# Performance work log

Measured on AMD Instinct MI355X. Metric: run time of the kernel, lower is better.

Reference implementation:

```python
import jax, jax.numpy as jnp
import numpy as np

D = 128        # node/time feature dim (n_node_features)
E = 20         # edge feature dim (hard-coded in TGS)
N = 4096       # number of source nodes
K = 10         # neighbors per node (hard-coded n_neighbors=10)
NUM_NODES = 100000
NUM_EDGES = 500000


def setup_inputs() -> dict:
    key = jax.random.key(0)
    ks = jax.random.split(key, 11)
    node_features = jax.random.normal(ks[0], (NUM_NODES, D), jnp.float32)
    edge_features = jax.random.normal(ks[1], (NUM_EDGES, E), jnp.float32)
    source_nodes = jax.random.randint(ks[2], (N,), 0, NUM_NODES)
    timestamps = jax.random.uniform(ks[3], (N,), jnp.float32) * 1000.0
    neighbors1 = jax.random.randint(ks[4], (N, K), 0, NUM_NODES)
    edge_idxs1 = jax.random.randint(ks[5], (N, K), 0, NUM_EDGES)
    edge_times1 = jax.random.uniform(ks[6], (N, K), jnp.float32) * 1000.0
    neighbors2 = jax.random.randint(ks[7], (N * K, K), 0, NUM_NODES)
    edge_idxs2 = jax.random.randint(ks[8], (N * K, K), 0, NUM_EDGES)
    edge_times2 = jax.random.uniform(ks[9], (N * K, K), jnp.float32) * 1000.0
    # TimeEncode params (TGN init: w = 1/10^linspace(0,9,D), b = 0)
    time_w = jnp.asarray(1.0 / 10.0 ** np.linspace(0, 9, D), jnp.float32)
    time_b = jnp.zeros((D,), jnp.float32)
    pk = jax.random.split(ks[10], 4)
    s1 = float(1.0 / np.sqrt(2 * D + E))
    lin1_w = jax.random.uniform(pk[0], (2, 2 * D + E, D), jnp.float32, -s1, s1)
    lin1_b = jax.random.uniform(pk[1], (2, D), jnp.float32, -s1, s1)
    s2 = float(1.0 / np.sqrt(3 * D))
    lin2_w = jax.random.uniform(pk[2], (2, 3 * D, D), jnp.float32, -s2, s2)
    lin2_b = jax.random.uniform(pk[3], (2, D), jnp.float32, -s2, s2)
    return dict(node_features=node_features, edge_features=edge_features,
                source_nodes=source_nodes, timestamps=timestamps,
                neighbors1=neighbors1, edge_idxs1=edge_idxs1, edge_times1=edge_times1,
                neighbors2=neighbors2, edge_idxs2=edge_idxs2, edge_times2=edge_times2,
                time_w=time_w, time_b=time_b,
                lin1_w=lin1_w, lin1_b=lin1_b, lin2_w=lin2_w, lin2_b=lin2_b)


def reference(node_features, edge_features, source_nodes, timestamps,
              neighbors1, edge_idxs1, edge_times1,
              neighbors2, edge_idxs2, edge_times2,
              time_w, time_b, lin1_w, lin1_b, lin2_w, lin2_b):
    def time_enc(t):
        # TGN TimeEncode: cos(t * w + b), broadcast over feature dim
        return jnp.cos(t[..., None] * time_w + time_b)

    def aggregate(layer, src_feat, src_time_emb, nbr_emb, edge_time_emb, edge_feat):
        # GraphSumEmbedding.aggregate
        nf = jnp.concatenate([nbr_emb, edge_time_emb, edge_feat], axis=-1)  # [n, K, 2D+E]
        h = nf @ lin1_w[layer] + lin1_b[layer]                              # [n, K, D]
        nbr_sum = jax.nn.relu(h.sum(axis=1))                                # [n, D]
        sf = jnp.concatenate([src_feat, src_time_emb, nbr_sum], axis=-1)   # [n, 3D]
        return sf @ lin2_w[layer] + lin2_b[layer]                           # [n, D]

    n, k = neighbors1.shape
    ts1 = jnp.repeat(timestamps, k)  # timestamps for the N*K first-hop neighbors

    # recursion level 1 (layer index 0): embed the N*K first-hop neighbors;
    # their neighbors' (level-0) embeddings are raw node features.
    emb1 = aggregate(
        0,
        node_features[neighbors1.reshape(-1)],          # [N*K, D]
        time_enc(jnp.zeros_like(ts1)),                  # [N*K, D]
        node_features[neighbors2],                      # [N*K, K, D]
        time_enc(ts1[:, None] - edge_times2),           # [N*K, K, D]
        edge_features[edge_idxs2])                      # [N*K, K, E]

    # recursion level 2 (layer index 1): embed the N source nodes
    emb2 = aggregate(
        1,
        node_features[source_nodes],                    # [N, D]
        time_enc(jnp.zeros_like(timestamps)),           # [N, D]
        emb1.reshape(n, k, -1),                         # [N, K, D]
        time_enc(timestamps[:, None] - edge_times1),    # [N, K, D]
        edge_features[edge_idxs1])                      # [N, K, E]
    return emb2
```

## Files before the change

### kernel.cpp

```cpp
#include <hip/hip_runtime.h>

#define TGS_D 128
#define TGS_E 20
#define TGS_K 10
#define TGS_F1 276
#define LDA1 296
#define LDA2 264
#define RPB 16

typedef _Float16 f16;
typedef _Float16 f16x4 __attribute__((ext_vector_type(4)));
typedef _Float16 f16x8 __attribute__((ext_vector_type(8)));
typedef float    f32x4 __attribute__((ext_vector_type(4)));

__global__ __launch_bounds__(256)
void tgs_nf16(const float* __restrict__ NF, f16* __restrict__ NF16) {
    const int i = (blockIdx.x * 256 + threadIdx.x) * 8;
    const float4 a = *(const float4*)(NF + i);
    const float4 b = *(const float4*)(NF + i + 4);
    *(f16x8*)(NF16 + i) = f16x8{(f16)a.x, (f16)a.y, (f16)a.z, (f16)a.w,
                                (f16)b.x, (f16)b.y, (f16)b.z, (f16)b.w};
}

__global__ __launch_bounds__(128)
void tgs_setup(const float* __restrict__ W1, const float* __restrict__ W2,
               const float* __restrict__ tb, const float* __restrict__ B2,
               f16x8* __restrict__ PW1, f16x8* __restrict__ PW2,
               float* __restrict__ tvec) {
    const int b = blockIdx.x, tid = threadIdx.x;
    if (b < 144) {
        if (tid < 64) {
            const int layer = b / 72, rem = b % 72, ntile = rem / 9, kk = rem % 9;
            const int colg = ntile * 16 + (tid & 15);
            const int kbase = kk * 32 + (tid >> 4) * 8;
            f16x8 v;
            #pragma unroll
            for (int j = 0; j < 8; ++j) {
                const int k = kbase + j;
                v[j] = (k < TGS_F1) ? (f16)W1[(layer * TGS_F1 + k) * TGS_D + colg] : (f16)0.f;
            }
            PW1[b * 64 + tid] = v;
        }
    } else if (b < 272) {
        if (tid < 64) {
            const int bb = b - 144;
            const int layer = bb / 64, rem = bb % 64, ntile = rem / 8, kk = rem % 8;
            const int colg = ntile * 16 + (tid & 15);
            const int kbase = kk * 32 + (tid >> 4) * 8;
            f16x8 v;
            #pragma unroll
            for (int j = 0; j < 8; ++j) {
                const int k = kbase + j;
                const int w2row = (k < TGS_D) ? k : (k + TGS_D);
                v[j] = (f16)W2[(layer * 3 * TGS_D + w2row) * TGS_D + colg];
            }
            PW2[bb * 64 + tid] = v;
        }
    } else {
        const int l = b - 272, d = tid;
        const float* w = W2 + (l * 3 * TGS_D + TGS_D) * TGS_D;
        float acc = B2[l * TGS_D + d];
        for (int j = 0; j < TGS_D; ++j)
            acc = fmaf(__cosf(tb[j]), w[j * TGS_D + d], acc);
        tvec[l * TGS_D + d] = acc;
    }
}

template<int LEVEL>
__global__ __launch_bounds__(256, 2)
void tgs_agg_kernel(
    const f16* __restrict__ NF16, const float* __restrict__ EF,
    const int* __restrict__ src_ids, const float* __restrict__ ts_arr,
    const int* __restrict__ nbr_idx,
    const int* __restrict__ eidx, const float* __restrict__ etime,
    const float* __restrict__ emb_in,
    const float* __restrict__ tw, const float* __restrict__ tb,
    const f16x8* __restrict__ PW1, const float* __restrict__ B1,
    const f16x8* __restrict__ PW2, const float* __restrict__ tvec,
    float* __restrict__ out)
{
    __shared__ f16 snf[RPB][LDA1];
    __shared__ f16 sf2[RPB][LDA2];
    __shared__ int   s_nbr[RPB * TGS_K];
    __shared__ int   s_eid[RPB * TGS_K];
    __shared__ float s_et [RPB * TGS_K];
    __shared__ float s_ts [RPB];

    const int tid = threadIdx.x;
    const int base_row = blockIdx.x * RPB;

    if (tid < RPB * TGS_K) {
        if (LEVEL == 1) s_nbr[tid] = nbr_idx[base_row * TGS_K + tid];
        s_eid[tid] = eidx[base_row * TGS_K + tid];
        s_et [tid] = etime[base_row * TGS_K + tid];
    }
    if (tid < RPB)
        s_ts[tid] = (LEVEL == 1) ? ts_arr[(base_row + tid) / TGS_K] : ts_arr[base_row + tid];
    __syncthreads();

    {
        const int sub = tid & 15;
        const int r   = tid >> 4;
        const int row = base_row + r;

        float a[8] = {0.f, 0.f, 0.f, 0.f, 0.f, 0.f, 0.f, 0.f};
        if (LEVEL == 1) {
            f16x8 vv[10];
            #pragma unroll
            for (int k = 0; k < TGS_K; ++k) {
                const int nb = s_nbr[r * TGS_K + k];
                vv[k] = *(const f16x8*)(NF16 + nb * TGS_D + sub * 8);
            }
            #pragma unroll
            for (int k = 0; k < TGS_K; ++k)
                #pragma unroll
                for (int j = 0; j < 8; ++j) a[j] += (float)vv[k][j];
        } else {
            float4 t[10];
            #pragma unroll
            for (int k = 0; k < TGS_K; ++k)
                t[k] = *(const float4*)(emb_in + (row * TGS_K + k) * TGS_D + sub * 8);
            #pragma unroll
            for (int k = 0; k < TGS_K; ++k) {
                a[0] += t[k].x; a[1] += t[k].y; a[2] += t[k].z; a[3] += t[k].w;
            }
            #pragma unroll
            for (int k = 0; k < TGS_K; ++k)
                t[k] = *(const float4*)(emb_in + (row * TGS_K + k) * TGS_D + sub * 8 + 4);
            #pragma unroll
            for (int k = 0; k < TGS_K; ++k) {
                a[4] += t[k].x; a[5] += t[k].y; a[6] += t[k].z; a[7] += t[k].w;
            }
        }
        f16x8 av;
        #pragma unroll
        for (int j = 0; j < 8; ++j) av[j] = (f16)a[j];
        *(f16x8*)&snf[r][sub * 8] = av;

        const int sid = src_ids[row];
        *(f16x8*)&sf2[r][sub * 8] = *(const f16x8*)(NF16 + sid * TGS_D + sub * 8);

        if (sub < 5) {
            float4 ev[10];
            #pragma unroll
            for (int k = 0; k < TGS_K; ++k)
                ev[k] = ((const float4*)(EF + s_eid[r * TGS_K + k] * TGS_E))[sub];
            float4 e = make_float4(0.f, 0.f, 0.f, 0.f);
            #pragma unroll
            for (int k = 0; k < TGS_K; ++k) {
                e.x += ev[k].x; e.y += ev[k].y; e.z += ev[k].z; e.w += ev[k].w;
            }
            *(f16x4*)&snf[r][2 * TGS_D + sub * 4] = f16x4{(f16)e.x, (f16)e.y, (f16)e.z, (f16)e.w};
        } else if (sub < 8) {
            *(f16x4*)&snf[r][2 * TGS_D + sub * 4] =
                f16x4{(f16)0.f, (f16)0.f, (f16)0.f, (f16)0.f};
        }

        const float4 w0 = ((const float4*)tw)[sub * 2];
        const float4 w1 = ((const float4*)tw)[sub * 2 + 1];
        const float4 b0 = ((const float4*)tb)[sub * 2];
        const float4 b1 = ((const float4*)tb)[sub * 2 + 1];
        const float ts = s_ts[r];
        float st[8] = {0.f, 0.f, 0.f, 0.f, 0.f, 0.f, 0.f, 0.f};
        #pragma unroll
        for (int k = 0; k < TGS_K; ++k) {
            const float dt = ts - s_et[r * TGS_K + k];
            st[0] += __cosf(fmaf(dt, w0.x, b0.x));
            st[1] += __cosf(fmaf(dt, w0.y, b0.y));
            st[2] += __cosf(fmaf(dt, w0.z, b0.z));
            st[3] += __cosf(fmaf(dt, w0.w, b0.w));
            st[4] += __cosf(fmaf(dt, w1.x, b1.x));
            st[5] += __cosf(fmaf(dt, w1.y, b1.y));
            st[6] += __cosf(fmaf(dt, w1.z, b1.z));
            st[7] += __cosf(fmaf(dt, w1.w, b1.w));
        }
        f16x8 sv;
        #pragma unroll
        for (int j = 0; j < 8; ++j) sv[j] = (f16)st[j];
        *(f16x8*)&snf[r][TGS_D + sub * 8] = sv;
    }
    __syncthreads();

    const int lane = tid & 63;
    const int w    = tid >> 6;
    const int ccol = lane & 15;
    const int row0 = (lane >> 4) * 4;

    {
        const int t0 = 2 * w, t1 = 2 * w + 1;
        f16x8 bfa[9], bfb[9];
        #pragma unroll
        for (int kk = 0; kk < 9; ++kk) {
            bfa[kk] = PW1[(t0 * 9 + kk) * 64 + lane];
            bfb[kk] = PW1[(t1 * 9 + kk) * 64 + lane];
        }
        f32x4 acc0 = {0.f, 0.f, 0.f, 0.f}, acc1 = acc0;
        const f16* abase = &snf[ccol][(lane >> 4) * 8];
        #pragma unroll
        for (int kk = 0; kk < 9; ++kk) {
            const f16x8 af = *(const f16x8*)(abase + kk * 32);
            acc0 = __builtin_amdgcn_mfma_f32_16x16x32_f16(af, bfa[kk], acc0, 0, 0, 0);
            acc1 = __builtin_amdgcn_mfma_f32_16x16x32_f16(af, bfb[kk], acc1, 0, 0, 0);
        }
        const float b1v0 = 10.f * B1[t0 * 16 + ccol];
        const float b1v1 = 10.f * B1[t1 * 16 + ccol];
        #pragma unroll
        for (int i = 0; i < 4; ++i) {
            sf2[row0 + i][TGS_D + t0 * 16 + ccol] = (f16)fmaxf(acc0[i] + b1v0, 0.f);
            sf2[row0 + i][TGS_D + t1 * 16 + ccol] = (f16)fmaxf(acc1[i] + b1v1, 0.f);
        }
    }
    __syncthreads();

    {
        const int t0 = 2 * w, t1 = 2 * w + 1;
        f16x8 bfa[8], bfb[8];
        #pragma unroll
        for (int kk = 0; kk < 8; ++kk) {
            bfa[kk] = PW2[(t0 * 8 + kk) * 64 + lane];
            bfb[kk] = PW2[(t1 * 8 + kk) * 64 + lane];
        }
        f32x4 acc0 = {0.f, 0.f, 0.f, 0.f}, acc1 = acc0;
        const f16* abase = &sf2[ccol][(lane >> 4) * 8];
        #pragma unroll
        for (int kk = 0; kk < 8; ++kk) {
            const f16x8 af = *(const f16x8*)(abase + kk * 32);
            acc0 = __builtin_amdgcn_mfma_f32_16x16x32_f16(af, bfa[kk], acc0, 0, 0, 0);
            acc1 = __builtin_amdgcn_mfma_f32_16x16x32_f16(af, bfb[kk], acc1, 0, 0, 0);
        }
        const float tv0 = tvec[t0 * 16 + ccol];
        const float tv1 = tvec[t1 * 16 + ccol];
        #pragma unroll
        for (int i = 0; i < 4; ++i) {
            out[(base_row + row0 + i) * TGS_D + t0 * 16 + ccol] = acc0[i] + tv0;
            out[(base_row + row0 + i) * TGS_D + t1 * 16 + ccol] = acc1[i] + tv1;
        }
    }
}

extern "C" void kernel_launch(void* const* d_in, const int* in_sizes, int n_in,
                              void* d_out, int out_size, void* d_ws, size_t ws_size,
                              hipStream_t stream) {
    const float* NF   = (const float*)d_in[0];
    const float* EF   = (const float*)d_in[1];
    const int*   SRC  = (const int*)  d_in[2];
    const float* TS   = (const float*)d_in[3];
    const int*   NBR1 = (const int*)  d_in[4];
    const int*   EI1  = (const int*)  d_in[5];
    const float* ET1  = (const float*)d_in[6];
    const int*   NBR2 = (const int*)  d_in[7];
    const int*   EI2  = (const int*)  d_in[8];
    const float* ET2  = (const float*)d_in[9];
    const float* TW   = (const float*)d_in[10];
    const float* TB   = (const float*)d_in[11];
    const float* W1   = (const float*)d_in[12];
    const float* B1   = (const float*)d_in[13];
    const float* W2   = (const float*)d_in[14];
    const float* B2   = (const float*)d_in[15];

    float* emb1 = (float*)d_ws;
    f16*   NF16 = (f16*)((char*)d_ws + 20971520);
    char*  wsb  = (char*)d_ws + 20971520 + 25600000;
    f16x8* PW1  = (f16x8*)wsb;
    f16x8* PW2  = (f16x8*)(wsb + 147456);
    float* tvec = (float*)(wsb + 147456 + 131072);

    tgs_nf16 <<<6250, 256, 0, stream>>>(NF, NF16);
    tgs_setup<<<274, 128, 0, stream>>>(W1, W2, TB, B2, PW1, PW2, tvec);

    const int n1 = 4096 * TGS_K;
    const int n2 = 4096;

    tgs_agg_kernel<1><<<n1 / RPB, 256, 0, stream>>>(
        NF16, EF, NBR1, TS, NBR2, EI2, ET2, nullptr,
        TW, TB, PW1, B1, PW2, tvec, emb1);

    tgs_agg_kernel<2><<<n2 / RPB, 256, 0, stream>>>(
        NF16, EF, SRC, TS, nullptr, EI1, ET1, emb1,
        TW, TB,
        PW1 + 8 * 9 * 64, B1 + TGS_D,
        PW2 + 8 * 8 * 64, tvec + TGS_D,
        (float*)d_out);
}
```

Baseline: 73.10 us.

## Stage gathers via direct global-to-LDS loads and store level-1 embeddings as fp16

```diff
diff --git a/kernel.cpp b/kernel.cpp
--- a/kernel.cpp
+++ b/kernel.cpp
@@ -5,13 +5,19 @@
 #define TGS_K 10
 #define TGS_F1 276
 #define LDA1 296
-#define LDA2 264
+#define LDH 136
 #define RPB 16
 
 typedef _Float16 f16;
 typedef _Float16 f16x4 __attribute__((ext_vector_type(4)));
 typedef _Float16 f16x8 __attribute__((ext_vector_type(8)));
 typedef float    f32x4 __attribute__((ext_vector_type(4)));
+
+__device__ __forceinline__ void gl_lds16(const void* g, void* l) {
+    __builtin_amdgcn_global_load_lds(
+        (const __attribute__((address_space(1))) char*)g,
+        (__attribute__((address_space(3))) char*)l, 16, 0, 0);
+}
 
 __global__ __launch_bounds__(256)
 void tgs_nf16(const float* __restrict__ NF, f16* __restrict__ NF16) {
@@ -73,20 +79,26 @@
     const int* __restrict__ src_ids, const float* __restrict__ ts_arr,
     const int* __restrict__ nbr_idx,
     const int* __restrict__ eidx, const float* __restrict__ etime,
-    const float* __restrict__ emb_in,
+    const f16* __restrict__ emb_in,
     const float* __restrict__ tw, const float* __restrict__ tb,
     const f16x8* __restrict__ PW1, const float* __restrict__ B1,
     const f16x8* __restrict__ PW2, const float* __restrict__ tvec,
-    float* __restrict__ out)
+    void* __restrict__ out_p)
 {
-    __shared__ f16 snf[RPB][LDA1];
-    __shared__ f16 sf2[RPB][LDA2];
+    __shared__ f16   stg[RPB * TGS_K * TGS_D];
+    __shared__ float stg_ef[832 * 4];
+    __shared__ f16   s_src[RPB * TGS_D];
+    __shared__ f16   snf[RPB][LDA1];
+    __shared__ f16   s_h[RPB][LDH];
     __shared__ int   s_nbr[RPB * TGS_K];
     __shared__ int   s_eid[RPB * TGS_K];
     __shared__ float s_et [RPB * TGS_K];
+    __shared__ int   s_sid[RPB];
     __shared__ float s_ts [RPB];
 
-    const int tid = threadIdx.x;
+    const int tid  = threadIdx.x;
+    const int lane = tid & 63;
+    const int wid  = tid >> 6;
     const int base_row = blockIdx.x * RPB;
 
     if (tid < RPB * TGS_K) {
@@ -94,68 +106,40 @@
         s_eid[tid] = eidx[base_row * TGS_K + tid];
         s_et [tid] = etime[base_row * TGS_K + tid];
     }
-    if (tid < RPB)
-        s_ts[tid] = (LEVEL == 1) ? ts_arr[(base_row + tid) / TGS_K] : ts_arr[base_row + tid];
+    if (tid < RPB) {
+        s_sid[tid] = src_ids[base_row + tid];
+        s_ts [tid] = (LEVEL == 1) ? ts_arr[(base_row + tid) / TGS_K] : ts_arr[base_row + tid];
+    }
     __syncthreads();
 
-    {
-        const int sub = tid & 15;
-        const int r   = tid >> 4;
-        const int row = base_row + r;
-
-        float a[8] = {0.f, 0.f, 0.f, 0.f, 0.f, 0.f, 0.f, 0.f};
-        if (LEVEL == 1) {
-            f16x8 vv[10];
-            #pragma unroll
-            for (int k = 0; k < TGS_K; ++k) {
-                const int nb = s_nbr[r * TGS_K + k];
-                vv[k] = *(const f16x8*)(NF16 + nb * TGS_D + sub * 8);
-            }
-            #pragma unroll
-            for (int k = 0; k < TGS_K; ++k)
-                #pragma unroll
-                for (int j = 0; j < 8; ++j) a[j] += (float)vv[k][j];
-        } else {
-            float4 t[10];
-            #pragma unroll
-            for (int k = 0; k < TGS_K; ++k)
-                t[k] = *(const float4*)(emb_in + (row * TGS_K + k) * TGS_D + sub * 8);
-            #pragma unroll
-            for (int k = 0; k < TGS_K; ++k) {
-                a[0] += t[k].x; a[1] += t[k].y; a[2] += t[k].z; a[3] += t[k].w;
-            }
-            #pragma unroll
-            for (int k = 0; k < TGS_K; ++k)
-                t[k] = *(const float4*)(emb_in + (row * TGS_K + k) * TGS_D + sub * 8 + 4);
-            #pragma unroll
-            for (int k = 0; k < TGS_K; ++k) {
-                a[4] += t[k].x; a[5] += t[k].y; a[6] += t[k].z; a[7] += t[k].w;
-            }
-        }
-        f16x8 av;
-        #pragma unroll
-        for (int j = 0; j < 8; ++j) av[j] = (f16)a[j];
-        *(f16x8*)&snf[r][sub * 8] = av;
-
-        const int sid = src_ids[row];
-        *(f16x8*)&sf2[r][sub * 8] = *(const f16x8*)(NF16 + sid * TGS_D + sub * 8);
-
-        if (sub < 5) {
-            float4 ev[10];
-            #pragma unroll
-            for (int k = 0; k < TGS_K; ++k)
-                ev[k] = ((const float4*)(EF + s_eid[r * TGS_K + k] * TGS_E))[sub];
-            float4 e = make_float4(0.f, 0.f, 0.f, 0.f);
-            #pragma unroll
-            for (int k = 0; k < TGS_K; ++k) {
-                e.x += ev[k].x; e.y += ev[k].y; e.z += ev[k].z; e.w += ev[k].w;
-            }
-            *(f16x4*)&snf[r][2 * TGS_D + sub * 4] = f16x4{(f16)e.x, (f16)e.y, (f16)e.z, (f16)e.w};
-        } else if (sub < 8) {
-            *(f16x4*)&snf[r][2 * TGS_D + sub * 4] =
-                f16x4{(f16)0.f, (f16)0.f, (f16)0.f, (f16)0.f};
-        }
-
+    #pragma unroll
+    for (int i = 0; i < 10; ++i) {
+        const int c  = wid * 640 + i * 64 + lane;
+        const int er = c >> 4, sub = c & 15;
+        const f16* g = (LEVEL == 1)
+            ? NF16 + s_nbr[er] * TGS_D + sub * 8
+            : emb_in + base_row * (TGS_K * TGS_D) + c * 8;
+        gl_lds16(g, (char*)stg + (wid * 640 + i * 64) * 16);
+    }
+    {
+        const int c = wid * 64 + lane;
+        const int r = c >> 4, slot = c & 15;
+        const f16* g = NF16 + s_sid[r] * TGS_D + (slot ^ r) * 8;
+        gl_lds16(g, (char*)s_src + wid * 1024);
+    }
+    #pragma unroll
+    for (int i = 0; i < 4; ++i) {
+        const int issue = i * 4 + wid;
+        if (issue < 13) {
+            const int c  = issue * 64 + lane;
+            const int ce = (c < 800) ? c : 0;
+            const int er = ce / 5, j = ce % 5;
+            gl_lds16(EF + s_eid[er] * TGS_E + j * 4, (char*)stg_ef + issue * 1024);
+        }
+    }
+
+    {
+        const int sub = tid & 15, r = tid >> 4;
         const float4 w0 = ((const float4*)tw)[sub * 2];
         const float4 w1 = ((const float4*)tw)[sub * 2 + 1];
         const float4 b0 = ((const float4*)tb)[sub * 2];
@@ -178,16 +162,42 @@
         #pragma unroll
         for (int j = 0; j < 8; ++j) sv[j] = (f16)st[j];
         *(f16x8*)&snf[r][TGS_D + sub * 8] = sv;
+        if (sub >= 5 && sub < 8)
+            *(f16x4*)&snf[r][2 * TGS_D + sub * 4] = f16x4{(f16)0.f, (f16)0.f, (f16)0.f, (f16)0.f};
     }
     __syncthreads();
 
-    const int lane = tid & 63;
-    const int w    = tid >> 6;
+    {
+        const int sub = tid & 15, r = tid >> 4;
+        float a[8] = {0.f, 0.f, 0.f, 0.f, 0.f, 0.f, 0.f, 0.f};
+        #pragma unroll
+        for (int k = 0; k < TGS_K; ++k) {
+            const f16x8 v = *(const f16x8*)&stg[((r * TGS_K + k) * 16 + sub) * 8];
+            #pragma unroll
+            for (int j = 0; j < 8; ++j) a[j] += (float)v[j];
+        }
+        f16x8 av;
+        #pragma unroll
+        for (int j = 0; j < 8; ++j) av[j] = (f16)a[j];
+        *(f16x8*)&snf[r][sub * 8] = av;
+
+        if (sub < 5) {
+            float4 e = make_float4(0.f, 0.f, 0.f, 0.f);
+            #pragma unroll
+            for (int k = 0; k < TGS_K; ++k) {
+                const float4 v = *(const float4*)&stg_ef[((r * TGS_K + k) * 5 + sub) * 4];
+                e.x += v.x; e.y += v.y; e.z += v.z; e.w += v.w;
+            }
+            *(f16x4*)&snf[r][2 * TGS_D + sub * 4] = f16x4{(f16)e.x, (f16)e.y, (f16)e.z, (f16)e.w};
+        }
+    }
+    __syncthreads();
+
     const int ccol = lane & 15;
     const int row0 = (lane >> 4) * 4;
-
-    {
-        const int t0 = 2 * w, t1 = 2 * w + 1;
+    const int t0 = 2 * wid, t1 = 2 * wid + 1;
+
+    {
         f16x8 bfa[9], bfb[9];
         #pragma unroll
         for (int kk = 0; kk < 9; ++kk) {
@@ -206,14 +216,13 @@
         const float b1v1 = 10.f * B1[t1 * 16 + ccol];
         #pragma unroll
         for (int i = 0; i < 4; ++i) {
-            sf2[row0 + i][TGS_D + t0 * 16 + ccol] = (f16)fmaxf(acc0[i] + b1v0, 0.f);
-            sf2[row0 + i][TGS_D + t1 * 16 + ccol] = (f16)fmaxf(acc1[i] + b1v1, 0.f);
+            s_h[row0 + i][t0 * 16 + ccol] = (f16)fmaxf(acc0[i] + b1v0, 0.f);
+            s_h[row0 + i][t1 * 16 + ccol] = (f16)fmaxf(acc1[i] + b1v1, 0.f);
         }
     }
     __syncthreads();
 
     {
-        const int t0 = 2 * w, t1 = 2 * w + 1;
         f16x8 bfa[8], bfb[8];
         #pragma unroll
         for (int kk = 0; kk < 8; ++kk) {
@@ -221,19 +230,37 @@
             bfb[kk] = PW2[(t1 * 8 + kk) * 64 + lane];
         }
         f32x4 acc0 = {0.f, 0.f, 0.f, 0.f}, acc1 = acc0;
-        const f16* abase = &sf2[ccol][(lane >> 4) * 8];
         #pragma unroll
         for (int kk = 0; kk < 8; ++kk) {
-            const f16x8 af = *(const f16x8*)(abase + kk * 32);
+            f16x8 af;
+            if (kk < 4) {
+                const int q = kk * 4 + (lane >> 4);
+                af = *(const f16x8*)&s_src[ccol * 16 * 8 + (q ^ ccol) * 8];
+            } else {
+                af = *(const f16x8*)&s_h[ccol][(kk - 4) * 32 + (lane >> 4) * 8];
+            }
             acc0 = __builtin_amdgcn_mfma_f32_16x16x32_f16(af, bfa[kk], acc0, 0, 0, 0);
             acc1 = __builtin_amdgcn_mfma_f32_16x16x32_f16(af, bfb[kk], acc1, 0, 0, 0);
         }
         const float tv0 = tvec[t0 * 16 + ccol];
         const float tv1 = tvec[t1 * 16 + ccol];
-        #pragma unroll
-        for (int i = 0; i < 4; ++i) {
-            out[(base_row + row0 + i) * TGS_D + t0 * 16 + ccol] = acc0[i] + tv0;
-            out[(base_row + row0 + i) * TGS_D + t1 * 16 + ccol] = acc1[i] + tv1;
+        if (LEVEL == 1) {
+            f16* s_out = &snf[0][0];
+            #pragma unroll
+            for (int i = 0; i < 4; ++i) {
+                s_out[(row0 + i) * TGS_D + t0 * 16 + ccol] = (f16)(acc0[i] + tv0);
+                s_out[(row0 + i) * TGS_D + t1 * 16 + ccol] = (f16)(acc1[i] + tv1);
+            }
+            __syncthreads();
+            f16* emb_out = (f16*)out_p;
+            *(f16x8*)&emb_out[base_row * TGS_D + tid * 8] = *(const f16x8*)&s_out[tid * 8];
+        } else {
+            float* outf = (float*)out_p;
+            #pragma unroll
+            for (int i = 0; i < 4; ++i) {
+                outf[(base_row + row0 + i) * TGS_D + t0 * 16 + ccol] = acc0[i] + tv0;
+                outf[(base_row + row0 + i) * TGS_D + t1 * 16 + ccol] = acc1[i] + tv1;
+            }
         }
     }
 }
@@ -258,12 +285,12 @@
     const float* W2   = (const float*)d_in[14];
     const float* B2   = (const float*)d_in[15];
 
-    float* emb1 = (float*)d_ws;
-    f16*   NF16 = (f16*)((char*)d_ws + 20971520);
-    char*  wsb  = (char*)d_ws + 20971520 + 25600000;
-    f16x8* PW1  = (f16x8*)wsb;
-    f16x8* PW2  = (f16x8*)(wsb + 147456);
-    float* tvec = (float*)(wsb + 147456 + 131072);
+    f16*   emb16 = (f16*)d_ws;
+    f16*   NF16  = (f16*)((char*)d_ws + 10485760);
+    char*  wsb   = (char*)d_ws + 10485760 + 25600000;
+    f16x8* PW1   = (f16x8*)wsb;
+    f16x8* PW2   = (f16x8*)(wsb + 147456);
+    float* tvec  = (float*)(wsb + 147456 + 131072);
 
     tgs_nf16 <<<6250, 256, 0, stream>>>(NF, NF16);
     tgs_setup<<<274, 128, 0, stream>>>(W1, W2, TB, B2, PW1, PW2, tvec);
@@ -272,13 +299,13 @@
     const int n2 = 4096;
 
     tgs_agg_kernel<1><<<n1 / RPB, 256, 0, stream>>>(
-        NF16, EF, NBR1, TS, NBR2, EI2, ET2, nullptr,
-        TW, TB, PW1, B1, PW2, tvec, emb1);
+        NF16, EF, NBR1, TS, NBR2, EI2, ET2, (const f16*)nullptr,
+        TW, TB, PW1, B1, PW2, tvec, emb16);
 
     tgs_agg_kernel<2><<<n2 / RPB, 256, 0, stream>>>(
-        NF16, EF, SRC, TS, nullptr, EI1, ET1, emb1,
+        NF16, EF, SRC, TS, nullptr, EI1, ET1, emb16,
         TW, TB,
         PW1 + 8 * 9 * 64, B1 + TGS_D,
         PW2 + 8 * 8 * 64, tvec + TGS_D,
-        (float*)d_out);
-}
+        d_out);
+}
```

New measurement: 77.17 us. +5.6%, slower.
